# Optimization experiments

Measured on AMD Instinct MI355X. Metric: run time of the kernel, lower is better.

Reference implementation:

```python
import jax, jax.numpy as jnp
import numpy as np

B, S, D = 2, 2048, 1024
H, HD = 16, 64          # num_heads, head_dim
K = 32                  # JL n_components


def setup_inputs() -> dict:
    key = jax.random.key(0)
    k1, k2, k3, k4 = jax.random.split(key, 4)
    return {
        "hidden_states": jax.random.normal(k1, (B, S, D), dtype=jnp.float32),
        "W_attn": jax.random.normal(k2, (D, 3 * D), dtype=jnp.float32) * 0.02,
        "b_attn": jnp.zeros((3 * D,), dtype=jnp.float32),
        "S_proj": jax.random.normal(k3, (K, HD), dtype=jnp.float32) / np.sqrt(K),
        "W_proj": jax.random.normal(k4, (D, D), dtype=jnp.float32) * 0.02,
        "b_proj": jnp.zeros((D,), dtype=jnp.float32),
    }


def reference(hidden_states, W_attn, b_attn, S_proj, W_proj, b_proj):
    b, s, d = hidden_states.shape
    # GPT2 Conv1D: x @ W + b, then split into q,k,v
    qkv = hidden_states @ W_attn + b_attn            # [B,S,3D]
    q, k, v = jnp.split(qkv, 3, axis=-1)
    # split heads -> [B,H,S,HD]
    def split_heads(x):
        return x.reshape(b, s, H, HD).transpose(0, 2, 1, 3)
    q = split_heads(q) @ S_proj.T                    # [B,H,S,K] JL-reduced
    k = split_heads(k) @ S_proj.T                    # [B,H,S,K]
    v = split_heads(v)                               # [B,H,S,HD]
    # naive attention: scale by sqrt(value head_dim) per GPT2 _attn
    scores = jnp.einsum("bhqk,bhsk->bhqs", q, k) / jnp.sqrt(
        jnp.asarray(HD, dtype=v.dtype))              # [B,H,S,S]
    causal = jnp.tril(jnp.ones((s, s), dtype=bool))
    mask_value = jnp.finfo(scores.dtype).min
    scores = jnp.where(causal, scores, mask_value)
    attn = jax.nn.softmax(scores, axis=-1)
    out = jnp.einsum("bhqs,bhsd->bhqd", attn, v)     # [B,H,S,HD]
    out = out.transpose(0, 2, 1, 3).reshape(b, s, d)  # merge heads
    return out @ W_proj + b_proj
```

## Files before the change

### kernel.cpp

```cpp
#include <hip/hip_runtime.h>
#include <hip/hip_bf16.h>
#include <stdint.h>

#define B_ 2
#define S_ 2048
#define D_ 1024
#define H_ 16
#define HD_ 64
#define KJL 32
#define N3 3072
#define N2 2048

typedef __attribute__((ext_vector_type(8))) __bf16 bf16x8;
typedef __attribute__((ext_vector_type(4))) float floatx4;
typedef __attribute__((ext_vector_type(4))) short short4v;
typedef __attribute__((ext_vector_type(2))) unsigned int uint2v;

__device__ __forceinline__ unsigned short f2b(float x) {
  union { float f; unsigned u; } v; v.f = x;
  unsigned r = v.u + 0x7fffu + ((v.u >> 16) & 1u);
  return (unsigned short)(r >> 16);
}

__device__ __forceinline__ unsigned int pkbf(float lo, float hi) {
  union { float f; unsigned u; } a, b;
  a.f = lo; b.f = hi;
  return __builtin_amdgcn_perm(b.u + 0x8000u, a.u + 0x8000u, 0x07060302u);
}

__device__ __forceinline__ void async16(const void* g, void* l) {
  __builtin_amdgcn_global_load_lds((__attribute__((address_space(1))) void*)(g),
                                   (__attribute__((address_space(3))) void*)(l),
                                   16, 0, 0);
}

__global__ __launch_bounds__(256)
void prep_kernel(const float* __restrict__ hidden, unsigned short* __restrict__ hB,
                 const float* __restrict__ W_attn, const float* __restrict__ b_attn,
                 const float* __restrict__ Sp, const float* __restrict__ W_proj,
                 unsigned short* __restrict__ Bt2, unsigned short* __restrict__ WpT,
                 float* __restrict__ bias2) {
  __shared__ float shmem[2048];
  const int bid = blockIdx.x;
  const int tid = threadIdx.x;

  if (bid < 512) {
    const int n4 = (B_ * S_ * D_) / 4;
    int i = bid * 256 + tid;
    for (; i < n4; i += 512 * 256) {
      float4 v = *(const float4*)(hidden + 4 * (size_t)i);
      short4v o = {(short)f2b(v.x), (short)f2b(v.y), (short)f2b(v.z), (short)f2b(v.w)};
      *(short4v*)(hB + 4 * (size_t)i) = o;
    }
  } else if (bid < 2560) {
    const float* in;
    unsigned short* out;
    int Cs, local;
    if (bid < 1536) { local = bid - 512;  in = W_attn + 2048; out = Bt2 + 1024 * 1024; Cs = N3; }
    else            { local = bid - 1536; in = W_proj;        out = WpT;               Cs = D_; }
    float (*t)[33] = (float(*)[33])shmem;
    int c0 = (local & 31) * 32, r0 = (local >> 5) * 32;
    int tx = tid & 31, ty = tid >> 5;
    for (int j = 0; j < 32; j += 8)
      t[ty + j][tx] = in[(size_t)(r0 + ty + j) * Cs + c0 + tx];
    __syncthreads();
    for (int j = 0; j < 32; j += 8)
      out[(size_t)(c0 + ty + j) * D_ + r0 + tx] = f2b(t[tx][ty + j]);
  } else {
    const int lb = bid - 2560;
    const int part = lb >> 6;
    const int h = (lb >> 2) & 15;
    const int dc = lb & 3;
    for (int i = tid; i < 32 * 64; i += 256) shmem[i] = Sp[i];
    __syncthreads();
    const float scale = part ? 1.0f : 0.125f * 1.44269504f;
    const int d = dc * 256 + tid;
    float w[64];
    const float* src = W_attn + (size_t)d * N3 + part * D_ + h * 64;
    for (int j = 0; j < 16; ++j) {
      float4 v = *(const float4*)&src[j * 4];
      w[j * 4 + 0] = v.x; w[j * 4 + 1] = v.y; w[j * 4 + 2] = v.z; w[j * 4 + 3] = v.w;
    }
    const int nbase = part * 512 + h * 32;
    for (int kjl = 0; kjl < 32; ++kjl) {
      float acc = 0.f;
      for (int hd = 0; hd < 64; ++hd) acc += w[hd] * shmem[kjl * 64 + hd];
      Bt2[(size_t)(nbase + kjl) * D_ + d] = f2b(acc * scale);
    }
    if (dc == 0 && tid < 32) {
      float acc = 0.f;
      for (int hd = 0; hd < 64; ++hd) acc += b_attn[part * D_ + h * 64 + hd] * shmem[tid * 64 + hd];
      bias2[nbase + tid] = acc * scale;
    }
  }
}

__global__ __launch_bounds__(256, 2)
void qkv2_gemm_kernel(const unsigned short* __restrict__ A,
                      const unsigned short* __restrict__ Bt,
                      const float* __restrict__ b_attn,
                      const float* __restrict__ bias2,
                      unsigned short* __restrict__ Qjl,
                      unsigned short* __restrict__ Kjl,
                      unsigned short* __restrict__ Vc) {
  __shared__ __align__(16) unsigned short As[2][128 * 32];
  __shared__ __align__(16) unsigned short Bs[2][128 * 32];
  const int tid = threadIdx.x;
  const int lane = tid & 63, wv = tid >> 6;
  const int quad = lane >> 4, col = lane & 15;
  const int wm = wv >> 1, wn = wv & 1;
  const int m0 = blockIdx.y * 128, n0 = blockIdx.x * 128;

  floatx4 acc[4][4] = {};

  for (int kk = 0; kk < D_; kk += 64) {
    for (int it = 0; it < 4; ++it) {
      int c = it * 256 + tid;
      int ks = c >> 9, row = (c >> 2) & 127, kc = c & 3;
      async16(A + (size_t)(m0 + row) * D_ + kk + ks * 32 + kc * 8,
              (unsigned short*)As + c * 8);
    }
    for (int it = 0; it < 4; ++it) {
      int c = it * 256 + tid;
      int ks = c >> 9, row = (c >> 2) & 127, kc = c & 3;
      async16(Bt + (size_t)(n0 + row) * D_ + kk + ks * 32 + kc * 8,
              (unsigned short*)Bs + c * 8);
    }
    asm volatile("s_waitcnt vmcnt(0)" ::: "memory");
    __syncthreads();
    for (int ks = 0; ks < 2; ++ks) {
      bf16x8 af[4], bfr[4];
      for (int mt = 0; mt < 4; ++mt)
        af[mt] = *(const bf16x8*)&As[ks][(wm * 64 + mt * 16 + col) * 32 + quad * 8];
      for (int nt = 0; nt < 4; ++nt)
        bfr[nt] = *(const bf16x8*)&Bs[ks][(wn * 64 + nt * 16 + col) * 32 + quad * 8];
      for (int mt = 0; mt < 4; ++mt)
        for (int nt = 0; nt < 4; ++nt)
          acc[mt][nt] = __builtin_amdgcn_mfma_f32_16x16x32_bf16(
              af[mt], bfr[nt], acc[mt][nt], 0, 0, 0);
    }
    __syncthreads();
  }

  const int pq = n0 >> 9;
  for (int mt = 0; mt < 4; ++mt) {
    int gm0 = m0 + wm * 64 + mt * 16 + quad * 4;
    int b = gm0 >> 11, s = gm0 & (S_ - 1);
    for (int nt = 0; nt < 4; ++nt) {
      int gn = n0 + wn * 64 + nt * 16 + col;
      if (pq >= 2) {
        int vcol = gn - 1024;
        float bs = b_attn[2048 + vcol];
        int h = vcol >> 6, hd = vcol & 63;
        short4v vv;
        for (int i = 0; i < 4; ++i)
          vv[i] = (short)f2b(acc[mt][nt][i] + bs);
        size_t idx = ((((size_t)(b * H_ + h) * 64 + (s >> 5)) * 64 + hd) * 32 + (s & 31));
        *(short4v*)&Vc[idx] = vv;
      } else {
        float bs = bias2[gn];
        int gl = gn & 511;
        int h = gl >> 5, kjl = gl & 31;
        unsigned short* dst = pq ? Kjl : Qjl;
        size_t base = ((size_t)(b * H_ + h) * S_ + s) * KJL + kjl;
        for (int i = 0; i < 4; ++i)
          dst[base + (size_t)i * KJL] = f2b(acc[mt][nt][i] + bs);
      }
    }
  }
}

__global__ __launch_bounds__(256, 2)
void attn_kernel(const unsigned short* __restrict__ Qjl,
                 const unsigned short* __restrict__ Kjl,
                 const unsigned short* __restrict__ Vc,
                 float* __restrict__ Part) {
  __shared__ __align__(16) unsigned short Ps[4][32 * 136];
  const int tid = threadIdx.x;
  const int lane = tid & 63, wv = tid >> 6;
  const int quad = lane >> 4, l15 = lane & 15;

  const int blk = blockIdx.x;
  const int bh = blk & 31;
  const int g0 = (blk >> 5) & 7;
  const int half = (blk >> 8) & 1;
  const int g = (blk & 512) ? (15 - g0) : g0;
  const int t = 63 - (g * 4 + wv);

  unsigned short* Pw = &Ps[wv][0];
  const int lastc = t >> 2;
  const int nch = lastc + 1;
  const int kb = half ? ((nch + 1) >> 1) : 0;
  const int ke = half ? nch : ((nch + 1) >> 1);
  const int r = t & 3;

  const int laneK = l15 * KJL + quad * 8;
  const int laneV = l15 * 32 + quad * 8;
  const unsigned short* Kp = Kjl + (size_t)bh * S_ * KJL + laneK + (size_t)kb * 128 * KJL;
  const unsigned short* Vp = Vc + (size_t)bh * (64 * 64 * 32) + laneV + (size_t)kb * 8192;

  bf16x8 aq[2];
  for (int qn = 0; qn < 2; ++qn)
    aq[qn] = *(const bf16x8*)&Qjl[(size_t)(bh * S_ + t * 32 + qn * 16 + l15) * KJL + quad * 8];

  floatx4 o[4][2] = {};
  floatx4 psum[2] = {};
  const floatx4 zz = {0.f, 0.f, 0.f, 0.f};

  for (int kt = kb; kt < ke; ++kt) {
    bf16x8 ak[8];
    for (int sm = 0; sm < 8; ++sm)
      ak[sm] = *(const bf16x8*)&Kp[sm * (16 * KJL)];
    bf16x8 bv[4][4];
    for (int ks = 0; ks < 4; ++ks)
      for (int md = 0; md < 4; ++md)
        bv[ks][md] = *(const bf16x8*)&Vp[ks * 2048 + md * 512];
    Kp += 128 * KJL;
    Vp += 8192;

    floatx4 sc[8][2];
    for (int sm = 0; sm < 8; ++sm)
      for (int qn = 0; qn < 2; ++qn)
        sc[sm][qn] = __builtin_amdgcn_mfma_f32_16x16x32_bf16(ak[sm], aq[qn], zz, 0, 0, 0);

    if (kt == lastc) {
      for (int qn = 0; qn < 2; ++qn) {
        int qloc = r * 32 + qn * 16 + l15;
        for (int sm = 0; sm < 8; ++sm)
          for (int i = 0; i < 4; ++i)
            if (sm * 16 + quad * 4 + i > qloc) sc[sm][qn][i] = -1e30f;
      }
    }

    for (int qn = 0; qn < 2; ++qn) {
      for (int sm = 0; sm < 8; ++sm) {
        float p0 = __builtin_amdgcn_exp2f(sc[sm][qn][0]);
        float p1 = __builtin_amdgcn_exp2f(sc[sm][qn][1]);
        float p2 = __builtin_amdgcn_exp2f(sc[sm][qn][2]);
        float p3 = __builtin_amdgcn_exp2f(sc[sm][qn][3]);
        psum[qn][0] += p0; psum[qn][1] += p1;
        psum[qn][2] += p2; psum[qn][3] += p3;
        uint2v pk2 = {pkbf(p0, p1), pkbf(p2, p3)};
        *(uint2v*)&Pw[(qn * 16 + l15) * 136 + sm * 16 + quad * 4] = pk2;
      }
    }

    for (int ks = 0; ks < 4; ++ks) {
      bf16x8 bp[2];
      for (int qn = 0; qn < 2; ++qn)
        bp[qn] = *(const bf16x8*)&Pw[(qn * 16 + l15) * 136 + ks * 32 + quad * 8];
      for (int qn = 0; qn < 2; ++qn)
        for (int md = 0; md < 4; ++md)
          o[md][qn] = __builtin_amdgcn_mfma_f32_16x16x32_bf16(bv[ks][md], bp[qn], o[md][qn], 0, 0, 0);
    }
  }

  float l0 = psum[0][0] + psum[0][1] + psum[0][2] + psum[0][3];
  float l1 = psum[1][0] + psum[1][1] + psum[1][2] + psum[1][3];
  l0 += __shfl_xor(l0, 16, 64); l0 += __shfl_xor(l0, 32, 64);
  l1 += __shfl_xor(l1, 16, 64); l1 += __shfl_xor(l1, 32, 64);

  const int tile = bh * 64 + t;
  float* Pp = Part + ((size_t)(tile * 2 + half) * 9 * 64 + lane) * 4;
  for (int qn = 0; qn < 2; ++qn)
    for (int md = 0; md < 4; ++md)
      *(floatx4*)(Pp + (size_t)(qn * 4 + md) * 256) = o[md][qn];
  floatx4 lv = {l0, l1, 0.f, 0.f};
  *(floatx4*)(Pp + (size_t)8 * 256) = lv;
}

__global__ __launch_bounds__(256, 4)
void merge_kernel(const float* __restrict__ Part, unsigned short* __restrict__ AO) {
  __shared__ __align__(16) unsigned short Os[4][32 * 72];
  const int tid = threadIdx.x;
  const int lane = tid & 63, wv = tid >> 6;
  const int quad = lane >> 4, l15 = lane & 15;
  const int tile = blockIdx.x * 4 + wv;
  const int bh = tile >> 6, t = tile & 63;
  const int b = bh >> 4, h = bh & 15;

  const float* P0 = Part + ((size_t)(tile * 2 + 0) * 9 * 64 + lane) * 4;
  const float* P1 = Part + ((size_t)(tile * 2 + 1) * 9 * 64 + lane) * 4;
  floatx4 la = *(const floatx4*)(P0 + (size_t)8 * 256);
  floatx4 lb = *(const floatx4*)(P1 + (size_t)8 * 256);
  float inv0 = 1.f / (la[0] + lb[0]);
  float inv1 = 1.f / (la[1] + lb[1]);

  unsigned short* Pw = &Os[wv][0];
  for (int qn = 0; qn < 2; ++qn) {
    float inv = qn ? inv1 : inv0;
    for (int md = 0; md < 4; ++md) {
      floatx4 a = *(const floatx4*)(P0 + (size_t)(qn * 4 + md) * 256);
      floatx4 c = *(const floatx4*)(P1 + (size_t)(qn * 4 + md) * 256);
      uint2v t4 = {pkbf((a[0] + c[0]) * inv, (a[1] + c[1]) * inv),
                   pkbf((a[2] + c[2]) * inv, (a[3] + c[3]) * inv)};
      *(uint2v*)&Pw[(qn * 16 + l15) * 72 + md * 16 + quad * 4] = t4;
    }
  }
  asm volatile("s_waitcnt lgkmcnt(0)" ::: "memory");
  {
    int q = lane >> 1, hf = lane & 1;
    size_t gbase = ((size_t)(b * S_ + t * 32 + q)) * D_ + h * HD_ + hf * 32;
    for (int jj = 0; jj < 4; ++jj) {
      bf16x8 v = *(const bf16x8*)&Pw[q * 72 + hf * 32 + jj * 8];
      *(bf16x8*)&AO[gbase + jj * 8] = v;
    }
  }
}

__global__ __launch_bounds__(256, 2)
void proj_gemm_kernel(const unsigned short* __restrict__ A,
                      const unsigned short* __restrict__ Bt,
                      const float* __restrict__ bias,
                      float* __restrict__ out) {
  __shared__ __align__(16) unsigned short As[2][64 * 32];
  __shared__ __align__(16) unsigned short Bs[2][128 * 32];
  const int tid = threadIdx.x;
  const int lane = tid & 63, wv = tid >> 6;
  const int quad = lane >> 4, col = lane & 15;
  const int wm = wv >> 1, wn = wv & 1;
  const int m0 = blockIdx.y * 64, n0 = blockIdx.x * 128;

  floatx4 acc[2][4] = {};

  for (int kk = 0; kk < D_; kk += 64) {
    for (int it = 0; it < 2; ++it) {
      int c = it * 256 + tid;
      int ks = c >> 8, row = (c >> 2) & 63, kc = c & 3;
      async16(A + (size_t)(m0 + row) * D_ + kk + ks * 32 + kc * 8,
              (unsigned short*)As + c * 8);
    }
    for (int it = 0; it < 4; ++it) {
      int c = it * 256 + tid;
      int ks = c >> 9, row = (c >> 2) & 127, kc = c & 3;
      async16(Bt + (size_t)(n0 + row) * D_ + kk + ks * 32 + kc * 8,
              (unsigned short*)Bs + c * 8);
    }
    asm volatile("s_waitcnt vmcnt(0)" ::: "memory");
    __syncthreads();
    for (int ks = 0; ks < 2; ++ks) {
      bf16x8 af[2], bfr[4];
      for (int mt = 0; mt < 2; ++mt)
        af[mt] = *(const bf16x8*)&As[ks][(wm * 32 + mt * 16 + col) * 32 + quad * 8];
      for (int nt = 0; nt < 4; ++nt)
        bfr[nt] = *(const bf16x8*)&Bs[ks][(wn * 64 + nt * 16 + col) * 32 + quad * 8];
      for (int mt = 0; mt < 2; ++mt)
        for (int nt = 0; nt < 4; ++nt)
          acc[mt][nt] = __builtin_amdgcn_mfma_f32_16x16x32_bf16(
              af[mt], bfr[nt], acc[mt][nt], 0, 0, 0);
    }
    __syncthreads();
  }

  for (int mt = 0; mt < 2; ++mt) {
    int gm0 = m0 + wm * 32 + mt * 16 + quad * 4;
    for (int nt = 0; nt < 4; ++nt) {
      int gn = n0 + wn * 64 + nt * 16 + col;
      float bs = bias[gn];
      for (int i = 0; i < 4; ++i)
        out[(size_t)(gm0 + i) * D_ + gn] = acc[mt][nt][i] + bs;
    }
  }
}

extern "C" void kernel_launch(void* const* d_in, const int* in_sizes, int n_in,
                              void* d_out, int out_size, void* d_ws, size_t ws_size,
                              hipStream_t stream) {
  (void)in_sizes; (void)n_in; (void)out_size; (void)ws_size;
  const float* hidden = (const float*)d_in[0];
  const float* W_attn = (const float*)d_in[1];
  const float* b_attn = (const float*)d_in[2];
  const float* S_proj = (const float*)d_in[3];
  const float* W_proj = (const float*)d_in[4];
  const float* b_proj = (const float*)d_in[5];
  float* out = (float*)d_out;

  char* ws = (char*)d_ws;
  unsigned short* hB    = (unsigned short*)(ws);
  unsigned short* Bt2   = (unsigned short*)(ws + (8u << 20));
  unsigned short* WpT   = (unsigned short*)(ws + (12u << 20));
  float*          bias2 = (float*)         (ws + (14u << 20));
  unsigned short* Qjl   = (unsigned short*)(ws + (15u << 20));
  unsigned short* Kjl   = (unsigned short*)(ws + (19u << 20));
  unsigned short* Vc    = (unsigned short*)(ws + (23u << 20));
  unsigned short* AO    = (unsigned short*)(ws + (31u << 20));
  float*          Part  = (float*)         (ws + (40u << 20));

  prep_kernel<<<2688, 256, 0, stream>>>(hidden, hB, W_attn, b_attn, S_proj,
                                        W_proj, Bt2, WpT, bias2);
  qkv2_gemm_kernel<<<dim3(N2 / 128, (B_ * S_) / 128), 256, 0, stream>>>(
      hB, Bt2, b_attn, bias2, Qjl, Kjl, Vc);
  attn_kernel<<<1024, 256, 0, stream>>>(Qjl, Kjl, Vc, Part);
  merge_kernel<<<512, 256, 0, stream>>>(Part, AO);
  proj_gemm_kernel<<<dim3(D_ / 128, (B_ * S_) / 64), 256, 0, stream>>>(
      AO, WpT, b_proj, out);
}
```

Before: 190.6 us.

## Fuse split-KV merge into attention kernel via per-tile atomic counter

Removes the separate merge kernel launch. Each attention wave writes its partial output and then increments a per-tile counter with an atomic. The second finisher reads the other half's partial, normalizes and writes the bf16 attention output. Counters are zeroed by extra blocks in the prep kernel. This saves one kernel launch and a full reread pass, at the cost of a threadfence and an atomic per wave, plus extra tail work in the last-finishing waves.

After: 383.1 us. 2.01x slower.

```diff
diff --git a/kernel.cpp b/kernel.cpp
--- a/kernel.cpp
+++ b/kernel.cpp
@@ -39,7 +39,7 @@
                  const float* __restrict__ W_attn, const float* __restrict__ b_attn,
                  const float* __restrict__ Sp, const float* __restrict__ W_proj,
                  unsigned short* __restrict__ Bt2, unsigned short* __restrict__ WpT,
-                 float* __restrict__ bias2) {
+                 float* __restrict__ bias2, unsigned* __restrict__ cnt) {
   __shared__ float shmem[2048];
   const int bid = blockIdx.x;
   const int tid = threadIdx.x;
@@ -66,7 +66,7 @@
     __syncthreads();
     for (int j = 0; j < 32; j += 8)
       out[(size_t)(c0 + ty + j) * D_ + r0 + tx] = f2b(t[tx][ty + j]);
-  } else {
+  } else if (bid < 2688) {
     const int lb = bid - 2560;
     const int part = lb >> 6;
     const int h = (lb >> 2) & 15;
@@ -92,6 +92,9 @@
       for (int hd = 0; hd < 64; ++hd) acc += b_attn[part * D_ + h * 64 + hd] * shmem[tid * 64 + hd];
       bias2[nbase + tid] = acc * scale;
     }
+  } else {
+    int i = (bid - 2688) * 256 + tid;
+    if (i < 2048) cnt[i] = 0u;
   }
 }
 
@@ -174,7 +177,9 @@
 void attn_kernel(const unsigned short* __restrict__ Qjl,
                  const unsigned short* __restrict__ Kjl,
                  const unsigned short* __restrict__ Vc,
-                 float* __restrict__ Part) {
+                 float* __restrict__ Part,
+                 unsigned* __restrict__ cnt,
+                 unsigned short* __restrict__ AO) {
   __shared__ __align__(16) unsigned short Ps[4][32 * 136];
   const int tid = threadIdx.x;
   const int lane = tid & 63, wv = tid >> 6;
@@ -267,38 +272,29 @@
       *(floatx4*)(Pp + (size_t)(qn * 4 + md) * 256) = o[md][qn];
   floatx4 lv = {l0, l1, 0.f, 0.f};
   *(floatx4*)(Pp + (size_t)8 * 256) = lv;
-}
-
-__global__ __launch_bounds__(256, 4)
-void merge_kernel(const float* __restrict__ Part, unsigned short* __restrict__ AO) {
-  __shared__ __align__(16) unsigned short Os[4][32 * 72];
-  const int tid = threadIdx.x;
-  const int lane = tid & 63, wv = tid >> 6;
-  const int quad = lane >> 4, l15 = lane & 15;
-  const int tile = blockIdx.x * 4 + wv;
-  const int bh = tile >> 6, t = tile & 63;
-  const int b = bh >> 4, h = bh & 15;
-
-  const float* P0 = Part + ((size_t)(tile * 2 + 0) * 9 * 64 + lane) * 4;
-  const float* P1 = Part + ((size_t)(tile * 2 + 1) * 9 * 64 + lane) * 4;
-  floatx4 la = *(const floatx4*)(P0 + (size_t)8 * 256);
-  floatx4 lb = *(const floatx4*)(P1 + (size_t)8 * 256);
-  float inv0 = 1.f / (la[0] + lb[0]);
-  float inv1 = 1.f / (la[1] + lb[1]);
-
-  unsigned short* Pw = &Os[wv][0];
-  for (int qn = 0; qn < 2; ++qn) {
-    float inv = qn ? inv1 : inv0;
-    for (int md = 0; md < 4; ++md) {
-      floatx4 a = *(const floatx4*)(P0 + (size_t)(qn * 4 + md) * 256);
-      floatx4 c = *(const floatx4*)(P1 + (size_t)(qn * 4 + md) * 256);
-      uint2v t4 = {pkbf((a[0] + c[0]) * inv, (a[1] + c[1]) * inv),
-                   pkbf((a[2] + c[2]) * inv, (a[3] + c[3]) * inv)};
-      *(uint2v*)&Pw[(qn * 16 + l15) * 72 + md * 16 + quad * 4] = t4;
-    }
-  }
-  asm volatile("s_waitcnt lgkmcnt(0)" ::: "memory");
-  {
+
+  __threadfence();
+  unsigned old = 0;
+  if ((lane & 63) == 0) old = atomicAdd(&cnt[tile], 1u);
+  old = __shfl((int)old, 0, 64);
+  if (old == 1) {
+    __threadfence();
+    const float* Po = Part + ((size_t)(tile * 2 + (half ^ 1)) * 9 * 64 + lane) * 4;
+    floatx4 lo = *(const floatx4*)(Po + (size_t)8 * 256);
+    float inv0 = 1.f / (l0 + lo[0]);
+    float inv1 = 1.f / (l1 + lo[1]);
+    for (int qn = 0; qn < 2; ++qn) {
+      float inv = qn ? inv1 : inv0;
+      for (int md = 0; md < 4; ++md) {
+        floatx4 a = *(const floatx4*)(Po + (size_t)(qn * 4 + md) * 256);
+        floatx4 s0 = o[md][qn];
+        uint2v t4 = {pkbf((s0[0] + a[0]) * inv, (s0[1] + a[1]) * inv),
+                     pkbf((s0[2] + a[2]) * inv, (s0[3] + a[3]) * inv)};
+        *(uint2v*)&Pw[(qn * 16 + l15) * 72 + md * 16 + quad * 4] = t4;
+      }
+    }
+    asm volatile("s_waitcnt lgkmcnt(0)" ::: "memory");
+    const int b = bh >> 4, h = bh & 15;
     int q = lane >> 1, hf = lane & 1;
     size_t gbase = ((size_t)(b * S_ + t * 32 + q)) * D_ + h * HD_ + hf * 32;
     for (int jj = 0; jj < 4; ++jj) {
@@ -385,13 +381,13 @@
   unsigned short* Vc    = (unsigned short*)(ws + (23u << 20));
   unsigned short* AO    = (unsigned short*)(ws + (31u << 20));
   float*          Part  = (float*)         (ws + (40u << 20));
-
-  prep_kernel<<<2688, 256, 0, stream>>>(hidden, hB, W_attn, b_attn, S_proj,
-                                        W_proj, Bt2, WpT, bias2);
+  unsigned*       cnt   = (unsigned*)      (ws + (79u << 20));
+
+  prep_kernel<<<2696, 256, 0, stream>>>(hidden, hB, W_attn, b_attn, S_proj,
+                                        W_proj, Bt2, WpT, bias2, cnt);
   qkv2_gemm_kernel<<<dim3(N2 / 128, (B_ * S_) / 128), 256, 0, stream>>>(
       hB, Bt2, b_attn, bias2, Qjl, Kjl, Vc);
-  attn_kernel<<<1024, 256, 0, stream>>>(Qjl, Kjl, Vc, Part);
-  merge_kernel<<<512, 256, 0, stream>>>(Part, AO);
+  attn_kernel<<<1024, 256, 0, stream>>>(Qjl, Kjl, Vc, Part, cnt, AO);
   proj_gemm_kernel<<<dim3(D_ / 128, (B_ * S_) / 64), 256, 0, stream>>>(
       AO, WpT, b_proj, out);
 }
```

## Fuse split-K attention merge into attention kernel via in-block wave pairs

Applied to the files above, without the earlier changes.

Pairs of waves in each attention block now handle the two key-halves of the same query tile. One wave writes its partial output and row sums to shared memory, and the other combines them, normalizes and writes bf16 output directly. This removes the separate merge kernel launch and the global round trip of fp32 partials. In exchange it adds a block-wide barrier and changes how query tiles map to blocks, with two tiles per block instead of four.

After: 183.6 us, median of 2. 3.7% less time.

```diff
diff --git a/kernel.cpp b/kernel.cpp
--- a/kernel.cpp
+++ b/kernel.cpp
@@ -174,7 +174,7 @@
 void attn_kernel(const unsigned short* __restrict__ Qjl,
                  const unsigned short* __restrict__ Kjl,
                  const unsigned short* __restrict__ Vc,
-                 float* __restrict__ Part) {
+                 unsigned short* __restrict__ AO) {
   __shared__ __align__(16) unsigned short Ps[4][32 * 136];
   const int tid = threadIdx.x;
   const int lane = tid & 63, wv = tid >> 6;
@@ -182,16 +182,20 @@
 
   const int blk = blockIdx.x;
   const int bh = blk & 31;
-  const int g0 = (blk >> 5) & 7;
-  const int half = (blk >> 8) & 1;
-  const int g = (blk & 512) ? (15 - g0) : g0;
-  const int t = 63 - (g * 4 + wv);
+  const int u = blk >> 5;
+  const int a = u & 7;
+  const int g = (u & 8) ? (15 - a) : a;
+  const int rp = (u >> 4) & 1;
+  const int pairid = wv >> 1;
+  const int half = wv & 1;
+  const int t = g * 4 + rp * 2 + pairid;
+  const int b = bh >> 4, h = bh & 15;
 
   unsigned short* Pw = &Ps[wv][0];
-  const int lastc = t >> 2;
-  const int nch = lastc + 1;
+  const int nch = g + 1;
   const int kb = half ? ((nch + 1) >> 1) : 0;
   const int ke = half ? nch : ((nch + 1) >> 1);
+  const int lastc = nch - 1;
   const int r = t & 3;
 
   const int laneK = l15 * KJL + quad * 8;
@@ -260,45 +264,31 @@
   l0 += __shfl_xor(l0, 16, 64); l0 += __shfl_xor(l0, 32, 64);
   l1 += __shfl_xor(l1, 16, 64); l1 += __shfl_xor(l1, 32, 64);
 
-  const int tile = bh * 64 + t;
-  float* Pp = Part + ((size_t)(tile * 2 + half) * 9 * 64 + lane) * 4;
-  for (int qn = 0; qn < 2; ++qn)
-    for (int md = 0; md < 4; ++md)
-      *(floatx4*)(Pp + (size_t)(qn * 4 + md) * 256) = o[md][qn];
-  floatx4 lv = {l0, l1, 0.f, 0.f};
-  *(floatx4*)(Pp + (size_t)8 * 256) = lv;
-}
-
-__global__ __launch_bounds__(256, 4)
-void merge_kernel(const float* __restrict__ Part, unsigned short* __restrict__ AO) {
-  __shared__ __align__(16) unsigned short Os[4][32 * 72];
-  const int tid = threadIdx.x;
-  const int lane = tid & 63, wv = tid >> 6;
-  const int quad = lane >> 4, l15 = lane & 15;
-  const int tile = blockIdx.x * 4 + wv;
-  const int bh = tile >> 6, t = tile & 63;
-  const int b = bh >> 4, h = bh & 15;
-
-  const float* P0 = Part + ((size_t)(tile * 2 + 0) * 9 * 64 + lane) * 4;
-  const float* P1 = Part + ((size_t)(tile * 2 + 1) * 9 * 64 + lane) * 4;
-  floatx4 la = *(const floatx4*)(P0 + (size_t)8 * 256);
-  floatx4 lb = *(const floatx4*)(P1 + (size_t)8 * 256);
-  float inv0 = 1.f / (la[0] + lb[0]);
-  float inv1 = 1.f / (la[1] + lb[1]);
-
-  unsigned short* Pw = &Os[wv][0];
-  for (int qn = 0; qn < 2; ++qn) {
-    float inv = qn ? inv1 : inv0;
-    for (int md = 0; md < 4; ++md) {
-      floatx4 a = *(const floatx4*)(P0 + (size_t)(qn * 4 + md) * 256);
-      floatx4 c = *(const floatx4*)(P1 + (size_t)(qn * 4 + md) * 256);
-      uint2v t4 = {pkbf((a[0] + c[0]) * inv, (a[1] + c[1]) * inv),
-                   pkbf((a[2] + c[2]) * inv, (a[3] + c[3]) * inv)};
-      *(uint2v*)&Pw[(qn * 16 + l15) * 72 + md * 16 + quad * 4] = t4;
-    }
-  }
-  asm volatile("s_waitcnt lgkmcnt(0)" ::: "memory");
-  {
+  if (half) {
+    float* fp = (float*)Pw;
+    for (int qn = 0; qn < 2; ++qn)
+      for (int md = 0; md < 4; ++md)
+        *(floatx4*)(fp + (qn * 4 + md) * 256 + lane * 4) = o[md][qn];
+    fp[2048 + lane] = l0;
+    fp[2112 + lane] = l1;
+  }
+  __syncthreads();
+
+  if (!half) {
+    const float* fq = (const float*)(&Ps[wv | 1][0]);
+    float inv0 = 1.f / (l0 + fq[2048 + lane]);
+    float inv1 = 1.f / (l1 + fq[2112 + lane]);
+    for (int qn = 0; qn < 2; ++qn) {
+      float inv = qn ? inv1 : inv0;
+      for (int md = 0; md < 4; ++md) {
+        floatx4 p = *(const floatx4*)(fq + (qn * 4 + md) * 256 + lane * 4);
+        floatx4 s = o[md][qn];
+        uint2v t4 = {pkbf((s[0] + p[0]) * inv, (s[1] + p[1]) * inv),
+                     pkbf((s[2] + p[2]) * inv, (s[3] + p[3]) * inv)};
+        *(uint2v*)&Pw[(qn * 16 + l15) * 72 + md * 16 + quad * 4] = t4;
+      }
+    }
+    asm volatile("s_waitcnt lgkmcnt(0)" ::: "memory");
     int q = lane >> 1, hf = lane & 1;
     size_t gbase = ((size_t)(b * S_ + t * 32 + q)) * D_ + h * HD_ + hf * 32;
     for (int jj = 0; jj < 4; ++jj) {
@@ -384,14 +374,12 @@
   unsigned short* Kjl   = (unsigned short*)(ws + (19u << 20));
   unsigned short* Vc    = (unsigned short*)(ws + (23u << 20));
   unsigned short* AO    = (unsigned short*)(ws + (31u << 20));
-  float*          Part  = (float*)         (ws + (40u << 20));
 
   prep_kernel<<<2688, 256, 0, stream>>>(hidden, hB, W_attn, b_attn, S_proj,
                                         W_proj, Bt2, WpT, bias2);
   qkv2_gemm_kernel<<<dim3(N2 / 128, (B_ * S_) / 128), 256, 0, stream>>>(
       hB, Bt2, b_attn, bias2, Qjl, Kjl, Vc);
-  attn_kernel<<<1024, 256, 0, stream>>>(Qjl, Kjl, Vc, Part);
-  merge_kernel<<<512, 256, 0, stream>>>(Part, AO);
+  attn_kernel<<<1024, 256, 0, stream>>>(Qjl, Kjl, Vc, AO);
   proj_gemm_kernel<<<dim3(D_ / 128, (B_ * S_) / 64), 256, 0, stream>>>(
       AO, WpT, b_proj, out);
 }
```
